# Kernel tuning notes

Measured on AMD Instinct MI355X. Metric: run time of the kernel, lower is better.

## Reference

```python
import jax, jax.numpy as jnp
import numpy as np

DT = 0.005
BETA = 0.9
THR = 0.5
TAU_MIN = 0.02
TAU_STEP = 0.03
TAU_R = 0.002
SLOPE = 25.0  # snntorch fast_sigmoid default surrogate slope

@jax.custom_vjp
def spike_fn(x):
    return (x > 0).astype(x.dtype)

def _spike_fwd(x):
    return spike_fn(x), x

def _spike_bwd(x, g):
    return (g / (SLOPE * jnp.abs(x) + 1.0) ** 2,)

spike_fn.defvjp(_spike_fwd, _spike_bwd)

def setup_inputs() -> dict:
    key = jax.random.key(0)
    ks = jax.random.split(key, 8)
    T, NIN, H, NOUT, P = 1000, 4, 4096, 2, 16
    inv_sqrt_h = 1.0 / np.sqrt(H).astype(np.float32)
    return {
        "x": jax.random.normal(ks[0], (T, NIN + 2, 1), jnp.float32),
        "noise": jax.random.normal(ks[1], (T, H, 1), jnp.float32),
        "Win": jax.random.normal(ks[2], (H, NIN + 2), jnp.float32),
        "Wout": jax.random.normal(ks[3], (NOUT, H), jnp.float32) * inv_sqrt_h,
        "pin": jax.random.normal(ks[4], (H, P), jnp.float32) * inv_sqrt_h,
        "pout": jax.random.normal(ks[5], (H, P), jnp.float32) * inv_sqrt_h,
        "l": jax.random.normal(ks[6], (P,), jnp.float32) * inv_sqrt_h,
        "sigmoid_tau_d": jax.random.normal(ks[7], (H, 1), jnp.float32),
    }

def reference(x, noise, Win, Wout, pin, pout, l, sigmoid_tau_d):
    H = Win.shape[0]
    tau_d = jax.nn.sigmoid(sigmoid_tau_d) * TAU_STEP + TAU_MIN   # [H,1]
    Wr = (l * pin) @ pout.T                                      # [H,H] low-rank recurrent matrix
    decay_r = jnp.exp(jnp.asarray(-DT / TAU_R, x.dtype))         # scalar
    decay_d = jnp.exp(-DT / tau_d)                               # [H,1]
    s_gain = DT / (tau_d * TAU_R)                                # [H,1]

    def step(carry, inp):
        mem, r, s = carry
        xi, ni = inp
        I = Win @ xi + Wr @ r + ni / 10.0                        # [H,1]
        # snntorch Leaky, reset_mechanism='subtract': reset from incoming mem (detached)
        reset = jax.lax.stop_gradient(spike_fn(mem - THR))
        mem = BETA * mem + I - reset * THR
        spk = spike_fn(mem - THR)
        s = s * decay_r + s_gain * spk
        r = decay_d * r + DT * s
        return (mem, r, s), r

    z = jnp.zeros((H, 1), x.dtype)
    _, R = jax.lax.scan(step, (z, z, z), (x, noise))             # R: [T,H,1]
    y = jnp.einsum('oh,thj->toj', Wout, R)                       # [T,O,1]
    return y
```

## Files before the change

### kernel.cpp

```cpp
#include <hip/hip_runtime.h>
#include <math.h>

#define KB       4
#define NTHREADS 256
#define NW       4
#define HID      4096
#define HB       (HID / KB)
#define NPT      4
#define TT       1000
#define PP       16
#define SLOTW    24

#define BETA 0.9f
#define THRV 0.5f
#define DTV  0.005f

template<int CTRL>
__device__ __forceinline__ float dppx(float v) {
    return __int_as_float(__builtin_amdgcn_update_dpp(
        0, __float_as_int(v), CTRL, 0xF, 0xF, true));
}

__global__ __launch_bounds__(NTHREADS, 1)
void snn_kernel(const float* __restrict__ x,
                const float* __restrict__ noise,
                const float* __restrict__ Win,
                const float* __restrict__ Wout,
                const float* __restrict__ pin,
                const float* __restrict__ pout,
                const float* __restrict__ lvec,
                const float* __restrict__ stdv,
                float* __restrict__ out,
                unsigned long long* __restrict__ slots)
{
    const int b    = blockIdx.x;
    const int tid  = threadIdx.x;
    const int wave = tid >> 6;
    const int lane = tid & 63;
    const int h0   = b * HB + tid * NPT;

    const bool lb0 = (lane & 1) != 0;
    const bool lb1 = (lane & 2) != 0;
    const bool lb2 = (lane & 4) != 0;
    const bool lb3 = (lane & 8) != 0;

    const int rb0 = (b == 0) ? 1 : 0;
    const int rb1 = (b <= 1) ? 2 : 1;
    const int rb2 = (b <= 2) ? 3 : 2;

    __shared__ float part[NW][20];
    __shared__ float ubuf[NW][16];

    float lv[PP];
    #pragma unroll
    for (int p = 0; p < PP; p += 4) {
        float4 t4 = *(const float4*)&lvec[p];
        lv[p] = t4.x; lv[p+1] = t4.y; lv[p+2] = t4.z; lv[p+3] = t4.w;
    }
    float pl[NPT][PP], po[NPT][PP];
    #pragma unroll
    for (int j = 0; j < NPT; ++j) {
        #pragma unroll
        for (int p = 0; p < PP; p += 4) {
            float4 a = *(const float4*)&pin[(h0+j)*PP + p];
            pl[j][p]   = a.x*lv[p];   pl[j][p+1] = a.y*lv[p+1];
            pl[j][p+2] = a.z*lv[p+2]; pl[j][p+3] = a.w*lv[p+3];
            float4 e = *(const float4*)&pout[(h0+j)*PP + p];
            po[j][p]   = e.x; po[j][p+1] = e.y;
            po[j][p+2] = e.z; po[j][p+3] = e.w;
        }
    }
    float win[NPT][6];
    #pragma unroll
    for (int j = 0; j < NPT; ++j) {
        const float2* wr = (const float2*)&Win[(h0+j)*6];
        float2 wA = wr[0], wB = wr[1], wC = wr[2];
        win[j][0]=wA.x; win[j][1]=wA.y; win[j][2]=wB.x;
        win[j][3]=wB.y; win[j][4]=wC.x; win[j][5]=wC.y;
    }
    float4 woa = *(const float4*)&Wout[h0];
    float4 wob = *(const float4*)&Wout[HID + h0];

    float4 sd4 = *(const float4*)&stdv[h0];
    float dd[NPT], sg[NPT];
    {
        float sdv[4] = { sd4.x, sd4.y, sd4.z, sd4.w };
        #pragma unroll
        for (int j = 0; j < NPT; ++j) {
            float sig = 1.f / (1.f + expf(-sdv[j]));
            float tau = sig * 0.03f + 0.02f;
            dd[j] = expf(-DTV / tau);
            sg[j] = DTV / (tau * 0.002f);
        }
    }
    const float DECAY_R = expf(-2.5f);

    float mem[NPT], rr[NPT], ss[NPT];
    #pragma unroll
    for (int j = 0; j < NPT; ++j) { mem[j] = 0.f; rr[j] = 0.f; ss[j] = 0.f; }

    const float2* x2 = (const float2*)x;
    float4 nz = *(const float4*)&noise[h0];
    float2 xa = x2[0], xb = x2[1], xc = x2[2];

    float uu[16];
    #pragma unroll
    for (int p = 0; p < 16; ++p) uu[p] = 0.f;

    for (int t = 0; t <= TT; ++t) {
        float4 nz_n = nz; float2 xa_n = xa, xb_n = xb, xc_n = xc;
        if (t < TT - 1) {
            const int tn = t + 1;
            nz_n = *(const float4*)&noise[tn * HID + h0];
            xa_n = x2[tn*3]; xb_n = x2[tn*3+1]; xc_n = x2[tn*3+2];
        }

        if (t > 0) {
            const int par = t & 1;
            float pa[18];
            #pragma unroll
            for (int p = 0; p < PP; ++p)
                pa[p] = (po[0][p]*rr[0] + po[1][p]*rr[1])
                      + (po[2][p]*rr[2] + po[3][p]*rr[3]);
            pa[16] = (woa.x*rr[0] + woa.y*rr[1]) + (woa.z*rr[2] + woa.w*rr[3]);
            pa[17] = (wob.x*rr[0] + wob.y*rr[1]) + (wob.z*rr[2] + wob.w*rr[3]);

            float a1[8], yv;
            #pragma unroll
            for (int k = 0; k < 8; ++k) {
                float keep = lb0 ? pa[2*k+1] : pa[2*k];
                float send = lb0 ? pa[2*k]   : pa[2*k+1];
                a1[k] = keep + dppx<0xB1>(send);
            }
            {
                float keep = lb0 ? pa[17] : pa[16];
                float send = lb0 ? pa[16] : pa[17];
                yv = keep + dppx<0xB1>(send);
            }
            float a2[4];
            #pragma unroll
            for (int k = 0; k < 4; ++k) {
                float keep = lb1 ? a1[2*k+1] : a1[2*k];
                float send = lb1 ? a1[2*k]   : a1[2*k+1];
                a2[k] = keep + dppx<0x4E>(send);
            }
            yv += dppx<0x4E>(yv);
            float a3[2];
            #pragma unroll
            for (int k = 0; k < 2; ++k) {
                float keep = lb2 ? a2[2*k+1] : a2[2*k];
                float send = lb2 ? a2[2*k]   : a2[2*k+1];
                a3[k] = keep + __shfl_xor(send, 4, 64);
            }
            yv += __shfl_xor(yv, 4, 64);
            float uv;
            {
                float keep = lb3 ? a3[1] : a3[0];
                float send = lb3 ? a3[0] : a3[1];
                uv = keep + dppx<0x128>(send);
            }
            yv += dppx<0x128>(yv);
            uv += __shfl_xor(uv, 16, 64);
            uv += __shfl_xor(uv, 32, 64);
            yv += __shfl_xor(yv, 16, 64);
            yv += __shfl_xor(yv, 32, 64);

            if (lane < 18) part[wave][lane] = (lane < 16) ? uv : yv;
            __syncthreads();

            float bs = 0.f;
            if (lane < 18) {
                bs = (part[0][lane] + part[1][lane])
                   + (part[2][lane] + part[3][lane]);
            }

            if (wave == 0 && lane < 18) {
                union { float f; unsigned u; } cv; cv.f = bs;
                unsigned long long pk = ((unsigned long long)(unsigned)t << 32)
                                      | (unsigned long long)cv.u;
                __hip_atomic_store(&slots[(size_t)(par*KB + b)*SLOTW + lane], pk,
                                   __ATOMIC_RELAXED, __HIP_MEMORY_SCOPE_AGENT);
            }

            if (t < TT || b == 0) {
                float f0 = 0.f, f1 = 0.f, f2 = 0.f;
                if (lane < 18) {
                    const unsigned long long* p0 =
                        &slots[(size_t)(par*KB + rb0)*SLOTW + lane];
                    const unsigned long long* p1 =
                        &slots[(size_t)(par*KB + rb1)*SLOTW + lane];
                    const unsigned long long* p2 =
                        &slots[(size_t)(par*KB + rb2)*SLOTW + lane];
                    unsigned long long v0, v1, v2;
                    int spin = 0;
                    do {
                        v0 = __hip_atomic_load(p0, __ATOMIC_RELAXED,
                                               __HIP_MEMORY_SCOPE_AGENT);
                        v1 = __hip_atomic_load(p1, __ATOMIC_RELAXED,
                                               __HIP_MEMORY_SCOPE_AGENT);
                        v2 = __hip_atomic_load(p2, __ATOMIC_RELAXED,
                                               __HIP_MEMORY_SCOPE_AGENT);
                    } while ((((int)(v0 >> 32) != t) | ((int)(v1 >> 32) != t) |
                              ((int)(v2 >> 32) != t)) && ++spin < (1 << 20));
                    union { unsigned u; float f; } c0, c1, c2;
                    c0.u = (unsigned)v0; c1.u = (unsigned)v1; c2.u = (unsigned)v2;
                    f0 = c0.f; f1 = c1.f; f2 = c2.f;
                }
                float total = (b < 2) ? ((bs + f0) + (f1 + f2))
                                      : ((f0 + f1) + (f2 + bs));
                if (lane < 16) ubuf[wave][lane] = total;
                if (b == 0 && wave == 0 && lane >= 16 && lane < 18)
                    out[(t-1)*2 + (lane - 16)] = total;

                float4 u0 = *(const float4*)&ubuf[wave][0];
                float4 u1 = *(const float4*)&ubuf[wave][4];
                float4 u2 = *(const float4*)&ubuf[wave][8];
                float4 u3 = *(const float4*)&ubuf[wave][12];
                uu[0]=u0.x; uu[1]=u0.y; uu[2]=u0.z; uu[3]=u0.w;
                uu[4]=u1.x; uu[5]=u1.y; uu[6]=u1.z; uu[7]=u1.w;
                uu[8]=u2.x; uu[9]=u2.y; uu[10]=u2.z; uu[11]=u2.w;
                uu[12]=u3.x; uu[13]=u3.y; uu[14]=u3.z; uu[15]=u3.w;
            }
        }

        if (t < TT) {
            float nzv[4] = { nz.x, nz.y, nz.z, nz.w };
            #pragma unroll
            for (int j = 0; j < NPT; ++j) {
                float ra = pl[j][0]*uu[0];
                float rb2_ = pl[j][8]*uu[8];
                #pragma unroll
                for (int p = 1; p < 8; ++p) {
                    ra   += pl[j][p]*uu[p];
                    rb2_ += pl[j][p+8]*uu[p+8];
                }
                float rec = ra + rb2_;
                float xw = win[j][0]*xa.x + win[j][1]*xa.y
                         + win[j][2]*xb.x + win[j][3]*xb.y
                         + win[j][4]*xc.x + win[j][5]*xc.y;
                float I = (xw + rec) + nzv[j] / 10.0f;

                float rst = (mem[j] - THRV > 0.f) ? THRV : 0.f;
                mem[j] = BETA*mem[j] + I - rst;
                float spk = (mem[j] - THRV > 0.f) ? 1.f : 0.f;
                ss[j] = ss[j]*DECAY_R + sg[j]*spk;
                rr[j] = dd[j]*rr[j] + DTV*ss[j];
            }
            nz = nz_n; xa = xa_n; xb = xb_n; xc = xc_n;
        }
    }
}

extern "C" void kernel_launch(void* const* d_in, const int* in_sizes, int n_in,
                              void* d_out, int out_size, void* d_ws, size_t ws_size,
                              hipStream_t stream)
{
    const float* x     = (const float*)d_in[0];
    const float* noise = (const float*)d_in[1];
    const float* Win   = (const float*)d_in[2];
    const float* Wout  = (const float*)d_in[3];
    const float* pin   = (const float*)d_in[4];
    const float* pout  = (const float*)d_in[5];
    const float* l     = (const float*)d_in[6];
    const float* stdv  = (const float*)d_in[7];
    float* out = (float*)d_out;
    unsigned long long* slots = (unsigned long long*)d_ws;

    hipLaunchKernelGGL(snn_kernel, dim3(KB), dim3(NTHREADS), 0, stream,
                       x, noise, Win, Wout, pin, pout, l, stdv,
                       out, slots);
}
```

Before: 1.631 ms.

## Replace block barrier with per-wave global slots and pipelined batched polling

Each wave now publishes its own partial sums to a global slot, so the per-step __syncthreads and LDS block reduction go away. Every wave polls all 16 wave slots with two overlapped batches of inline-asm loads, and falls back to a plain spin loop if the pipelined poll stalls. The step is also split so that the spike-independent parts of the state update and projection are precomputed before the wait. Only the spike correction is added afterward, which shortens the critical path after the barrier. The cost is more global polling traffic (16 loads per lane instead of 3), fragile hand-written asm and waitcnt handling, and a changed floating-point summation order.

```diff
diff --git a/kernel.cpp b/kernel.cpp
--- a/kernel.cpp
+++ b/kernel.cpp
@@ -9,7 +9,8 @@
 #define NPT      4
 #define TT       1000
 #define PP       16
-#define SLOTW    24
+#define SLOTW    32
+#define NLINES   (KB * NW)
 
 #define BETA 0.9f
 #define THRV 0.5f
@@ -20,6 +21,50 @@
     return __int_as_float(__builtin_amdgcn_update_dpp(
         0, __float_as_int(v), CTRL, 0xF, 0xF, true));
 }
+
+__device__ __forceinline__ unsigned long long AL(const unsigned long long* p) {
+    return __hip_atomic_load(p, __ATOMIC_RELAXED, __HIP_MEMORY_SCOPE_AGENT);
+}
+__device__ __forceinline__ void AS(unsigned long long* p, unsigned long long v) {
+    __hip_atomic_store(p, v, __ATOMIC_RELAXED, __HIP_MEMORY_SCOPE_AGENT);
+}
+
+#define ISSUE16(B) asm volatile( \
+    "global_load_dwordx2 %0,  %16, %17 sc1\n\t" \
+    "global_load_dwordx2 %1,  %16, %17 offset:256 sc1\n\t" \
+    "global_load_dwordx2 %2,  %16, %17 offset:512 sc1\n\t" \
+    "global_load_dwordx2 %3,  %16, %17 offset:768 sc1\n\t" \
+    "global_load_dwordx2 %4,  %16, %17 offset:1024 sc1\n\t" \
+    "global_load_dwordx2 %5,  %16, %17 offset:1280 sc1\n\t" \
+    "global_load_dwordx2 %6,  %16, %17 offset:1536 sc1\n\t" \
+    "global_load_dwordx2 %7,  %16, %17 offset:1792 sc1\n\t" \
+    "global_load_dwordx2 %8,  %16, %17 offset:2048 sc1\n\t" \
+    "global_load_dwordx2 %9,  %16, %17 offset:2304 sc1\n\t" \
+    "global_load_dwordx2 %10, %16, %17 offset:2560 sc1\n\t" \
+    "global_load_dwordx2 %11, %16, %17 offset:2816 sc1\n\t" \
+    "global_load_dwordx2 %12, %16, %17 offset:3072 sc1\n\t" \
+    "global_load_dwordx2 %13, %16, %17 offset:3328 sc1\n\t" \
+    "global_load_dwordx2 %14, %16, %17 offset:3584 sc1\n\t" \
+    "global_load_dwordx2 %15, %16, %17 offset:3840 sc1" \
+    : "+v"(B[0]),  "+v"(B[1]),  "+v"(B[2]),  "+v"(B[3]), \
+      "+v"(B[4]),  "+v"(B[5]),  "+v"(B[6]),  "+v"(B[7]), \
+      "+v"(B[8]),  "+v"(B[9]),  "+v"(B[10]), "+v"(B[11]), \
+      "+v"(B[12]), "+v"(B[13]), "+v"(B[14]), "+v"(B[15]) \
+    : "v"(vo), "s"(slots) : "memory")
+
+#define WAIT16 do { asm volatile("s_waitcnt vmcnt(16)" ::: "memory"); \
+                    __builtin_amdgcn_sched_barrier(0); } while (0)
+
+#define PAY(v)   __uint_as_float((unsigned)(v))
+#define TAGOK(v) ((unsigned)((v) >> 32) == tw)
+#define CHECK16(B) (TAGOK(B[0])&TAGOK(B[1])&TAGOK(B[2])&TAGOK(B[3])& \
+                    TAGOK(B[4])&TAGOK(B[5])&TAGOK(B[6])&TAGOK(B[7])& \
+                    TAGOK(B[8])&TAGOK(B[9])&TAGOK(B[10])&TAGOK(B[11])& \
+                    TAGOK(B[12])&TAGOK(B[13])&TAGOK(B[14])&TAGOK(B[15]))
+#define TREE16(B) ((((PAY(B[0])+PAY(B[1]))+(PAY(B[2])+PAY(B[3]))) + \
+                    ((PAY(B[4])+PAY(B[5]))+(PAY(B[6])+PAY(B[7])))) + \
+                   (((PAY(B[8])+PAY(B[9]))+(PAY(B[10])+PAY(B[11]))) + \
+                    ((PAY(B[12])+PAY(B[13]))+(PAY(B[14])+PAY(B[15])))))
 
 __global__ __launch_bounds__(NTHREADS, 1)
 void snn_kernel(const float* __restrict__ x,
@@ -37,6 +82,7 @@
     const int tid  = threadIdx.x;
     const int wave = tid >> 6;
     const int lane = tid & 63;
+    const int Lown = b * NW + wave;
     const int h0   = b * HB + tid * NPT;
 
     const bool lb0 = (lane & 1) != 0;
@@ -44,11 +90,6 @@
     const bool lb2 = (lane & 4) != 0;
     const bool lb3 = (lane & 8) != 0;
 
-    const int rb0 = (b == 0) ? 1 : 0;
-    const int rb1 = (b <= 1) ? 2 : 1;
-    const int rb2 = (b <= 2) ? 3 : 2;
-
-    __shared__ float part[NW][20];
     __shared__ float ubuf[NW][16];
 
     float lv[PP];
@@ -65,9 +106,9 @@
             float4 a = *(const float4*)&pin[(h0+j)*PP + p];
             pl[j][p]   = a.x*lv[p];   pl[j][p+1] = a.y*lv[p+1];
             pl[j][p+2] = a.z*lv[p+2]; pl[j][p+3] = a.w*lv[p+3];
-            float4 e = *(const float4*)&pout[(h0+j)*PP + p];
-            po[j][p]   = e.x; po[j][p+1] = e.y;
-            po[j][p+2] = e.z; po[j][p+3] = e.w;
+            float4 e4 = *(const float4*)&pout[(h0+j)*PP + p];
+            po[j][p]   = e4.x; po[j][p+1] = e4.y;
+            po[j][p+2] = e4.z; po[j][p+3] = e4.w;
         }
     }
     float win[NPT][6];
@@ -94,10 +135,15 @@
         }
     }
     const float DECAY_R = expf(-2.5f);
+    const float DTE     = DTV * DECAY_R;
 
     float mem[NPT], rr[NPT], ss[NPT];
-    #pragma unroll
-    for (int j = 0; j < NPT; ++j) { mem[j] = 0.f; rr[j] = 0.f; ss[j] = 0.f; }
+    float pre[NPT], rlin[NPT], slin[NPT];
+    float palin[PP], yalin = 0.f, yblin = 0.f;
+    #pragma unroll
+    for (int j = 0; j < NPT; ++j) { mem[j]=0.f; rr[j]=0.f; ss[j]=0.f; }
+    #pragma unroll
+    for (int p = 0; p < PP; ++p) palin[p] = 0.f;
 
     const float2* x2 = (const float2*)x;
     float4 nz = *(const float4*)&noise[h0];
@@ -107,23 +153,126 @@
     #pragma unroll
     for (int p = 0; p < 16; ++p) uu[p] = 0.f;
 
+    float bpart = 0.f;
+    unsigned long long bat0[16] = {0}, bat1[16] = {0};
+    int use_pipe = 1;
+
     for (int t = 0; t <= TT; ++t) {
-        float4 nz_n = nz; float2 xa_n = xa, xb_n = xb, xc_n = xc;
-        if (t < TT - 1) {
-            const int tn = t + 1;
-            nz_n = *(const float4*)&noise[tn * HID + h0];
-            xa_n = x2[tn*3]; xb_n = x2[tn*3+1]; xc_n = x2[tn*3+2];
-        }
-
-        if (t > 0) {
-            const int par = t & 1;
+        const int par = t & 1;
+
+        if (t > 0 && lane < 18) {
+            union { float f; unsigned u; } cv; cv.f = bpart;
+            unsigned long long pk = ((unsigned long long)(unsigned)t << 32)
+                                  | (unsigned long long)cv.u;
+            AS(&slots[(size_t)(par*NLINES + Lown)*SLOTW + lane], pk);
+        }
+
+        if (t < TT) {
+            float nzv[4] = { nz.x, nz.y, nz.z, nz.w };
+            #pragma unroll
+            for (int j = 0; j < NPT; ++j) {
+                float xw = win[j][0]*xa.x + win[j][1]*xa.y
+                         + win[j][2]*xb.x + win[j][3]*xb.y
+                         + win[j][4]*xc.x + win[j][5]*xc.y;
+                float rst = (mem[j] - THRV > 0.f) ? THRV : 0.f;
+                pre[j]  = BETA*mem[j] + xw + nzv[j] / 10.0f - rst;
+                rlin[j] = dd[j]*rr[j] + DTE*ss[j];
+                slin[j] = DECAY_R*ss[j];
+            }
+            #pragma unroll
+            for (int p = 0; p < PP; ++p)
+                palin[p] = (po[0][p]*rlin[0] + po[1][p]*rlin[1])
+                         + (po[2][p]*rlin[2] + po[3][p]*rlin[3]);
+            yalin = (woa.x*rlin[0]+woa.y*rlin[1]) + (woa.z*rlin[2]+woa.w*rlin[3]);
+            yblin = (wob.x*rlin[0]+wob.y*rlin[1]) + (wob.z*rlin[2]+wob.w*rlin[3]);
+        }
+
+        if (t > 0 && (t < TT || b == 0)) {
+            const unsigned tw = (unsigned)t;
+            const unsigned vo = (unsigned)(par * (NLINES*SLOTW*8) + lane*8);
+            const bool act = (lane < 18);
+            float total = 0.f;
+            int got = act ? 0 : 1;
+
+            if (use_pipe) {
+                if (act) { ISSUE16(bat0); ISSUE16(bat1); }
+                const int CAP = (t == 1) ? 512 : 128;
+                int sp = 0, alldone = 0;
+                for (;;) {
+                    WAIT16;
+                    if (act && !got) {
+                        if (CHECK16(bat0)) { total = TREE16(bat0); got = 1; }
+                        else ISSUE16(bat0);
+                    }
+                    alldone = __all(got); if (alldone) break;
+                    WAIT16;
+                    if (act && !got) {
+                        if (CHECK16(bat1)) { total = TREE16(bat1); got = 1; }
+                        else ISSUE16(bat1);
+                    }
+                    alldone = __all(got); if (alldone) break;
+                    if (++sp >= CAP) break;
+                }
+                if (!alldone) {
+                    asm volatile("s_waitcnt vmcnt(0)" ::: "memory");
+                    use_pipe = 0;
+                }
+            }
+            if (!use_pipe && act && !got) {
+                const unsigned long long* bp =
+                    slots + (size_t)par*NLINES*SLOTW + lane;
+                int sp2 = 0;
+                for (;;) {
+                    unsigned long long v[16]; int ok = 1;
+                    #pragma unroll
+                    for (int L = 0; L < 16; ++L) {
+                        v[L] = AL(bp + (size_t)L*SLOTW);
+                        ok &= ((unsigned)(v[L] >> 32) == tw);
+                    }
+                    if (ok) { total = TREE16(v); break; }
+                    if (++sp2 >= (1 << 20)) break;
+                }
+            }
+
+            if (lane < 16) ubuf[wave][lane] = total;
+            if (b == 0 && wave == 0 && lane >= 16 && lane < 18)
+                out[(t-1)*2 + (lane - 16)] = total;
+
+            float4 u0 = *(const float4*)&ubuf[wave][0];
+            float4 u1 = *(const float4*)&ubuf[wave][4];
+            float4 u2 = *(const float4*)&ubuf[wave][8];
+            float4 u3 = *(const float4*)&ubuf[wave][12];
+            uu[0]=u0.x; uu[1]=u0.y; uu[2]=u0.z; uu[3]=u0.w;
+            uu[4]=u1.x; uu[5]=u1.y; uu[6]=u1.z; uu[7]=u1.w;
+            uu[8]=u2.x; uu[9]=u2.y; uu[10]=u2.z; uu[11]=u2.w;
+            uu[12]=u3.x; uu[13]=u3.y; uu[14]=u3.z; uu[15]=u3.w;
+        }
+
+        if (t < TT) {
+            float rs[NPT];
+            #pragma unroll
+            for (int j = 0; j < NPT; ++j) {
+                float ra  = pl[j][0]*uu[0];
+                float rb_ = pl[j][8]*uu[8];
+                #pragma unroll
+                for (int p = 1; p < 8; ++p) {
+                    ra  += pl[j][p]*uu[p];
+                    rb_ += pl[j][p+8]*uu[p+8];
+                }
+                mem[j] = pre[j] + (ra + rb_);
+                bool spk = (mem[j] - THRV > 0.f);
+                float rspk = spk ? DTV*sg[j] : 0.f;
+                ss[j] = slin[j] + (spk ? sg[j] : 0.f);
+                rr[j] = rlin[j] + rspk;
+                rs[j] = rspk;
+            }
             float pa[18];
             #pragma unroll
             for (int p = 0; p < PP; ++p)
-                pa[p] = (po[0][p]*rr[0] + po[1][p]*rr[1])
-                      + (po[2][p]*rr[2] + po[3][p]*rr[3]);
-            pa[16] = (woa.x*rr[0] + woa.y*rr[1]) + (woa.z*rr[2] + woa.w*rr[3]);
-            pa[17] = (wob.x*rr[0] + wob.y*rr[1]) + (wob.z*rr[2] + wob.w*rr[3]);
+                pa[p] = palin[p] + ((po[0][p]*rs[0] + po[1][p]*rs[1])
+                                 +  (po[2][p]*rs[2] + po[3][p]*rs[3]));
+            pa[16] = yalin + ((woa.x*rs[0]+woa.y*rs[1]) + (woa.z*rs[2]+woa.w*rs[3]));
+            pa[17] = yblin + ((wob.x*rs[0]+wob.y*rs[1]) + (wob.z*rs[2]+wob.w*rs[3]));
 
             float a1[8], yv;
             #pragma unroll
@@ -164,89 +313,13 @@
             uv += __shfl_xor(uv, 32, 64);
             yv += __shfl_xor(yv, 16, 64);
             yv += __shfl_xor(yv, 32, 64);
-
-            if (lane < 18) part[wave][lane] = (lane < 16) ? uv : yv;
-            __syncthreads();
-
-            float bs = 0.f;
-            if (lane < 18) {
-                bs = (part[0][lane] + part[1][lane])
-                   + (part[2][lane] + part[3][lane]);
-            }
-
-            if (wave == 0 && lane < 18) {
-                union { float f; unsigned u; } cv; cv.f = bs;
-                unsigned long long pk = ((unsigned long long)(unsigned)t << 32)
-                                      | (unsigned long long)cv.u;
-                __hip_atomic_store(&slots[(size_t)(par*KB + b)*SLOTW + lane], pk,
-                                   __ATOMIC_RELAXED, __HIP_MEMORY_SCOPE_AGENT);
-            }
-
-            if (t < TT || b == 0) {
-                float f0 = 0.f, f1 = 0.f, f2 = 0.f;
-                if (lane < 18) {
-                    const unsigned long long* p0 =
-                        &slots[(size_t)(par*KB + rb0)*SLOTW + lane];
-                    const unsigned long long* p1 =
-                        &slots[(size_t)(par*KB + rb1)*SLOTW + lane];
-                    const unsigned long long* p2 =
-                        &slots[(size_t)(par*KB + rb2)*SLOTW + lane];
-                    unsigned long long v0, v1, v2;
-                    int spin = 0;
-                    do {
-                        v0 = __hip_atomic_load(p0, __ATOMIC_RELAXED,
-                                               __HIP_MEMORY_SCOPE_AGENT);
-                        v1 = __hip_atomic_load(p1, __ATOMIC_RELAXED,
-                                               __HIP_MEMORY_SCOPE_AGENT);
-                        v2 = __hip_atomic_load(p2, __ATOMIC_RELAXED,
-                                               __HIP_MEMORY_SCOPE_AGENT);
-                    } while ((((int)(v0 >> 32) != t) | ((int)(v1 >> 32) != t) |
-                              ((int)(v2 >> 32) != t)) && ++spin < (1 << 20));
-                    union { unsigned u; float f; } c0, c1, c2;
-                    c0.u = (unsigned)v0; c1.u = (unsigned)v1; c2.u = (unsigned)v2;
-                    f0 = c0.f; f1 = c1.f; f2 = c2.f;
-                }
-                float total = (b < 2) ? ((bs + f0) + (f1 + f2))
-                                      : ((f0 + f1) + (f2 + bs));
-                if (lane < 16) ubuf[wave][lane] = total;
-                if (b == 0 && wave == 0 && lane >= 16 && lane < 18)
-                    out[(t-1)*2 + (lane - 16)] = total;
-
-                float4 u0 = *(const float4*)&ubuf[wave][0];
-                float4 u1 = *(const float4*)&ubuf[wave][4];
-                float4 u2 = *(const float4*)&ubuf[wave][8];
-                float4 u3 = *(const float4*)&ubuf[wave][12];
-                uu[0]=u0.x; uu[1]=u0.y; uu[2]=u0.z; uu[3]=u0.w;
-                uu[4]=u1.x; uu[5]=u1.y; uu[6]=u1.z; uu[7]=u1.w;
-                uu[8]=u2.x; uu[9]=u2.y; uu[10]=u2.z; uu[11]=u2.w;
-                uu[12]=u3.x; uu[13]=u3.y; uu[14]=u3.z; uu[15]=u3.w;
-            }
-        }
-
-        if (t < TT) {
-            float nzv[4] = { nz.x, nz.y, nz.z, nz.w };
-            #pragma unroll
-            for (int j = 0; j < NPT; ++j) {
-                float ra = pl[j][0]*uu[0];
-                float rb2_ = pl[j][8]*uu[8];
-                #pragma unroll
-                for (int p = 1; p < 8; ++p) {
-                    ra   += pl[j][p]*uu[p];
-                    rb2_ += pl[j][p+8]*uu[p+8];
-                }
-                float rec = ra + rb2_;
-                float xw = win[j][0]*xa.x + win[j][1]*xa.y
-                         + win[j][2]*xb.x + win[j][3]*xb.y
-                         + win[j][4]*xc.x + win[j][5]*xc.y;
-                float I = (xw + rec) + nzv[j] / 10.0f;
-
-                float rst = (mem[j] - THRV > 0.f) ? THRV : 0.f;
-                mem[j] = BETA*mem[j] + I - rst;
-                float spk = (mem[j] - THRV > 0.f) ? 1.f : 0.f;
-                ss[j] = ss[j]*DECAY_R + sg[j]*spk;
-                rr[j] = dd[j]*rr[j] + DTV*ss[j];
-            }
-            nz = nz_n; xa = xa_n; xb = xb_n; xc = xc_n;
+            bpart = (lane < 16) ? uv : yv;
+
+            if (t < TT - 1) {
+                const int tn = t + 1;
+                nz = *(const float4*)&noise[tn * HID + h0];
+                xa = x2[tn*3]; xb = x2[tn*3+1]; xc = x2[tn*3+2];
+            }
         }
     }
 }
```

New measurement: 2.461 ms. +50.9%, slower.
